# Performance work log

Hardware: AMD Instinct MI355X
Metric: run time of the kernel (lower is better)

## Reference

```python
import jax, jax.numpy as jnp
import numpy as np

C = 256  # in_dims
CQ = C // 2


def setup_inputs() -> dict:
    key = jax.random.key(0)
    ks = jax.random.split(key, 8)
    B, H, W = 8, 64, 64
    x = jax.random.normal(ks[0], (B, C, H, W), dtype=jnp.float32)
    s = 0.02
    Wq = jax.random.normal(ks[1], (CQ, C), dtype=jnp.float32) * s
    bq = jax.random.normal(ks[2], (CQ,), dtype=jnp.float32) * s
    Wk = jax.random.normal(ks[3], (CQ, C), dtype=jnp.float32) * s
    bk = jax.random.normal(ks[4], (CQ,), dtype=jnp.float32) * s
    Wv = jax.random.normal(ks[5], (C, C), dtype=jnp.float32) * s
    bv = jax.random.normal(ks[6], (C,), dtype=jnp.float32) * s
    gamma = jax.random.normal(ks[7], (1,), dtype=jnp.float32) * 0.5  # torch inits to 0; use nonzero for a meaningful test
    return {"x": x, "Wq": Wq, "bq": bq, "Wk": Wk, "bk": bk, "Wv": Wv, "bv": bv, "gamma": gamma}


def reference(x, Wq, bq, Wk, bk, Wv, bv, gamma):
    B, Ch, H, W = x.shape
    N = H * W
    xf = x.reshape(B, Ch, N)  # 1x1 conv == per-pixel linear over channels
    q = jnp.einsum('oc,bcn->bon', Wq, xf) + bq[None, :, None]  # [B, C/2, N]
    k = jnp.einsum('oc,bcn->bon', Wk, xf) + bk[None, :, None]  # [B, C/2, N]
    v = jnp.einsum('oc,bcn->bon', Wv, xf) + bv[None, :, None]  # [B, C,   N]
    # attention[b, m, n] = q_m . k_n ; softmax over dim=1 (the m axis), matching nn.Softmax(dim=1)
    scores = jnp.einsum('bcm,bcn->bmn', q, k)  # [B, N, N]
    attn = jax.nn.softmax(scores, axis=1)
    # torch.bmm(V, A^T)[b,c,m] = sum_n V[b,c,n] * A[b,m,n]
    out = jnp.einsum('bcn,bmn->bcm', v, attn)  # [B, C, N]
    return gamma * out.reshape(B, Ch, H, W) + x
```

## Files before the change

### kernel.cpp

```cpp
#include <hip/hip_runtime.h>


typedef unsigned short u16;
typedef __attribute__((ext_vector_type(8))) short bf16x8;
typedef __attribute__((ext_vector_type(4))) short bf16x4;
typedef __attribute__((ext_vector_type(4))) float f32x4;

__device__ __forceinline__ float bf2f(u16 u) {
  union { unsigned int i; float f; } v; v.i = ((unsigned int)u) << 16; return v.f;
}
__device__ __forceinline__ u16 f2bf(float f) {
  union { float f; unsigned int i; } v; v.f = f;
  unsigned int r = v.i + 0x7fffu + ((v.i >> 16) & 1u);
  return (u16)(r >> 16);
}

#define NB 8
#define NC 256
#define NCQ 128
#define NN 4096
#define LOG2E 1.4426950408889634f

__device__ __forceinline__ int scan_bad(const u16* p, int ns, int tid) {
  int bad = 0;
  for (int i = tid; i < ns; i += 256) {
    const int e = (p[2 * i] >> 7) & 0xff;
    bad |= (e >= 0x90) ? 1 : 0;
  }
  return bad;
}

__device__ __forceinline__ bf16x8 load8(const u16* pb, const float* pf,
                                        size_t off, bool f) {
  if (!f) return *(const bf16x8*)(pb + off);
  const float4 a = *(const float4*)(pf + off);
  const float4 b = *(const float4*)(pf + off + 4);
  bf16x8 r;
  r[0] = (short)f2bf(a.x); r[1] = (short)f2bf(a.y);
  r[2] = (short)f2bf(a.z); r[3] = (short)f2bf(a.w);
  r[4] = (short)f2bf(b.x); r[5] = (short)f2bf(b.y);
  r[6] = (short)f2bf(b.z); r[7] = (short)f2bf(b.w);
  return r;
}

__global__ __launch_bounds__(256, 2) void qkv_kernel(
    const void* xv, const void* Wqv, const void* bqv, const void* Wkv,
    const void* bkv, const void* Wvv, const void* bvv,
    u16* __restrict__ q2T, u16* __restrict__ kT, u16* __restrict__ vout) {
  __shared__ __align__(16) u16 xT[64][264];
  __shared__ int fl[8];
  const int tid = threadIdx.x;
  const int bid = blockIdx.x;
  const int b = bid & 7, n0 = (bid >> 3) << 6;

  if (tid < 8) fl[tid] = 0;
  __syncthreads();
  if (scan_bad((const u16*)xv, 256, tid)) fl[0] = 1;
  if (scan_bad((const u16*)Wqv, 64, tid)) fl[1] = 1;
  if (scan_bad((const u16*)Wkv, 64, tid)) fl[2] = 1;
  if (scan_bad((const u16*)Wvv, 64, tid)) fl[3] = 1;
  if (scan_bad((const u16*)bqv, 64, tid)) fl[4] = 1;
  if (scan_bad((const u16*)bkv, 64, tid)) fl[5] = 1;
  if (scan_bad((const u16*)bvv, 64, tid)) fl[6] = 1;
  __syncthreads();
  const bool fx = fl[0] != 0;

  {
    const int c = tid;
    const size_t roff = (size_t)(b * NC + c) * NN + n0;
    if (fx) {
      const float* xp = (const float*)xv + roff;
#pragma unroll
      for (int j = 0; j < 16; ++j) {
        const float4 t = *(const float4*)(xp + j * 4);
        xT[j * 4 + 0][c] = f2bf(t.x); xT[j * 4 + 1][c] = f2bf(t.y);
        xT[j * 4 + 2][c] = f2bf(t.z); xT[j * 4 + 3][c] = f2bf(t.w);
      }
    } else {
      const u16* xp = (const u16*)xv + roff;
#pragma unroll
      for (int j = 0; j < 8; ++j) {
        bf16x8 t = *(const bf16x8*)(xp + j * 8);
#pragma unroll
        for (int e = 0; e < 8; ++e) xT[j * 8 + e][c] = (u16)t[e];
      }
    }
  }
  __syncthreads();

  const int w = tid >> 6, lane = tid & 63, l15 = lane & 15, quad = lane >> 4;
  const u16* Wb; const float* Wf; const u16* Bb; const float* Bf;
  bool fW, fB; int obase = 0; u16* dstT = nullptr; float sc = 1.f;
  if (w == 0) {
    Wb = (const u16*)Wqv; Wf = (const float*)Wqv;
    Bb = (const u16*)bqv; Bf = (const float*)bqv;
    fW = fl[1]; fB = fl[4]; dstT = q2T; sc = LOG2E;
  } else if (w == 1) {
    Wb = (const u16*)Wkv; Wf = (const float*)Wkv;
    Bb = (const u16*)bkv; Bf = (const float*)bkv;
    fW = fl[2]; fB = fl[5]; dstT = kT;
  } else if (w == 2) {
    Wb = (const u16*)Wvv; Wf = (const float*)Wvv;
    Bb = (const u16*)bvv; Bf = (const float*)bvv;
    fW = fl[3]; fB = fl[6];
  } else {
    Wb = (const u16*)Wvv + 32768; Wf = (const float*)Wvv + 32768;
    Bb = (const u16*)bvv + 128;   Bf = (const float*)bvv + 128;
    fW = fl[3]; fB = fl[6]; obase = 128;
  }

  bf16x8 xfr[4][8];
#pragma unroll
  for (int nt = 0; nt < 4; ++nt) {
    const u16* xp = &xT[nt * 16 + l15][quad * 8];
#pragma unroll
    for (int ks = 0; ks < 8; ++ks) xfr[nt][ks] = *(const bf16x8*)(xp + ks * 32);
  }

  for (int ot = 0; ot < 8; ++ot) {
    bf16x8 wfr[8];
    const size_t wrow = (size_t)(ot * 16 + l15) * 256 + quad * 8;
#pragma unroll
    for (int ks = 0; ks < 8; ++ks) wfr[ks] = load8(Wb, Wf, wrow + ks * 32, fW);
    float bias[4];
    {
      const int boff = ot * 16 + quad * 4;
#pragma unroll
      for (int r = 0; r < 4; ++r)
        bias[r] = fB ? Bf[boff + r] : bf2f(Bb[boff + r]);
    }
#pragma unroll
    for (int nt = 0; nt < 4; ++nt) {
      f32x4 acc = {0.f, 0.f, 0.f, 0.f};
#pragma unroll
      for (int ks = 0; ks < 8; ++ks)
        acc = __builtin_amdgcn_mfma_f32_16x16x32_bf16(wfr[ks], xfr[nt][ks], acc, 0, 0, 0);
      const int n = n0 + nt * 16 + l15;
      if (w < 2) {
        ushort4 st;
        st.x = f2bf((acc[0] + bias[0]) * sc); st.y = f2bf((acc[1] + bias[1]) * sc);
        st.z = f2bf((acc[2] + bias[2]) * sc); st.w = f2bf((acc[3] + bias[3]) * sc);
        *(ushort4*)(dstT + ((size_t)(b * NN + n)) * NCQ + ot * 16 + quad * 4) = st;
      } else {
        const int c = obase + ot * 16 + quad * 4;
#pragma unroll
        for (int r = 0; r < 4; ++r)
          vout[((size_t)(b * NC + c + r)) * NN + n] = f2bf(acc[r] + bias[r]);
      }
    }
  }
}

__global__ __launch_bounds__(256, 2) void stats_kernel(
    const u16* __restrict__ q2T, const u16* __restrict__ kT,
    float* __restrict__ rbuf) {
  __shared__ __align__(16) u16 ksl[64][136];
  __shared__ float zbuf[4][64];
  const int bid = blockIdx.x;
  const int b = bid & 7, n0 = (bid >> 3) << 6;
  const int tid = threadIdx.x;
  const int w = tid >> 6, lane = tid & 63, l15 = lane & 15, quad = lane >> 4;

  {
    const int nn = tid >> 2, ck = (tid & 3) * 32;
    const u16* src = kT + ((size_t)(b * NN + n0 + nn)) * NCQ + ck;
#pragma unroll
    for (int j = 0; j < 4; ++j)
      *(bf16x8*)(&ksl[nn][ck + j * 8]) = *(const bf16x8*)(src + j * 8);
  }
  __syncthreads();

  float Z[4] = {0.f, 0.f, 0.f, 0.f};
  for (int it = 0; it < 64; ++it) {
    const int mb = w * 1024 + it * 16;
    const u16* qp = q2T + ((size_t)(b * NN + mb + l15)) * NCQ + quad * 8;
    bf16x8 af[4];
#pragma unroll
    for (int ks = 0; ks < 4; ++ks) af[ks] = *(const bf16x8*)(qp + ks * 32);
#pragma unroll
    for (int nt = 0; nt < 4; ++nt) {
      f32x4 acc = {0.f, 0.f, 0.f, 0.f};
#pragma unroll
      for (int ks = 0; ks < 4; ++ks) {
        const bf16x8 kfr = *(const bf16x8*)(&ksl[nt * 16 + l15][quad * 8 + ks * 32]);
        acc = __builtin_amdgcn_mfma_f32_16x16x32_bf16(af[ks], kfr, acc, 0, 0, 0);
      }
      Z[nt] += __builtin_amdgcn_exp2f(acc[0]) + __builtin_amdgcn_exp2f(acc[1]) +
               __builtin_amdgcn_exp2f(acc[2]) + __builtin_amdgcn_exp2f(acc[3]);
    }
  }
#pragma unroll
  for (int nt = 0; nt < 4; ++nt) {
    float z = Z[nt];
    z += __shfl_xor(z, 16, 64);
    z += __shfl_xor(z, 32, 64);
    Z[nt] = z;
  }
  if (lane < 16) {
#pragma unroll
    for (int nt = 0; nt < 4; ++nt) zbuf[w][nt * 16 + lane] = Z[nt];
  }
  __syncthreads();
  if (tid < 64) {
    const float z = zbuf[0][tid] + zbuf[1][tid] + zbuf[2][tid] + zbuf[3][tid];
    rbuf[b * NN + n0 + tid] = 1.0f / z;
  }
}

__global__ __launch_bounds__(256, 4) void scale_kernel(
    u16* __restrict__ vr, const float* __restrict__ rbuf) {
  const int flat = (blockIdx.x * 256 + threadIdx.x) * 8;
  const int n = flat & (NN - 1);
  const int b = flat >> 20;
  const float4 r0 = *(const float4*)(rbuf + (b << 12) + n);
  const float4 r1 = *(const float4*)(rbuf + (b << 12) + n + 4);
  const ushort4 a0 = *(const ushort4*)(vr + flat);
  const ushort4 a1 = *(const ushort4*)(vr + flat + 4);
  ushort4 s0, s1;
  s0.x = f2bf(bf2f(a0.x) * r0.x); s0.y = f2bf(bf2f(a0.y) * r0.y);
  s0.z = f2bf(bf2f(a0.z) * r0.z); s0.w = f2bf(bf2f(a0.w) * r0.w);
  s1.x = f2bf(bf2f(a1.x) * r1.x); s1.y = f2bf(bf2f(a1.y) * r1.y);
  s1.z = f2bf(bf2f(a1.z) * r1.z); s1.w = f2bf(bf2f(a1.w) * r1.w);
  *(ushort4*)(vr + flat) = s0;
  *(ushort4*)(vr + flat + 4) = s1;
}

__global__ __launch_bounds__(256, 4) void out_kernel(
    const u16* __restrict__ q2T, const u16* __restrict__ kT,
    const u16* __restrict__ vr,
    const void* xv, const void* gv,
    const void* bqv, const void* bkv, const void* bvv,
    void* outv) {
  __shared__ __align__(16) u16 qs[64][136];
  __shared__ __align__(16) u16 et[2][4][16][68];
  __shared__ int fl[2];
  const int tid = threadIdx.x;
  if (tid < 2) fl[tid] = 0;
  __syncthreads();
  if (scan_bad((const u16*)xv, 256, tid)) fl[0] = 1;
  if (scan_bad((const u16*)bqv, 64, tid) | scan_bad((const u16*)bkv, 64, tid) |
      scan_bad((const u16*)bvv, 64, tid)) fl[1] = 1;

  const int bid = blockIdx.x;
  const int b = bid & 7;
  const int r7 = bid >> 3;
  const int ch = r7 & 1;
  const int m0 = (r7 >> 1) << 6;
  const int w = tid >> 6, lane = tid & 63, l15 = lane & 15, quad = lane >> 4;

  {
    const int mm = tid >> 2, ck = (tid & 3) * 32;
    const u16* src = q2T + ((size_t)(b * NN + m0 + mm)) * NCQ + ck;
#pragma unroll
    for (int j = 0; j < 4; ++j)
      *(bf16x8*)(&qs[mm][ck + j * 8]) = *(const bf16x8*)(src + j * 8);
  }
  __syncthreads();
  const bool fx = fl[0] != 0, fg = fl[1] != 0;

  f32x4 acc[8];
#pragma unroll
  for (int i = 0; i < 8; ++i) acc[i] = (f32x4){0.f, 0.f, 0.f, 0.f};

  const u16* kb = kT + ((size_t)(b * NN + w * 16 + l15)) * NCQ + quad * 8;
  const u16* vb = vr + ((size_t)(b * NC + ch * 128 + w * 32 + l15)) * NN + quad * 8;

  for (int n0 = 0; n0 < NN; n0 += 64) {
    const int pp = (n0 >> 6) & 1;
    bf16x8 kf[4], vf[4];
#pragma unroll
    for (int ks = 0; ks < 4; ++ks)
      kf[ks] = *(const bf16x8*)(kb + (size_t)n0 * NCQ + ks * 32);
#pragma unroll
    for (int ct = 0; ct < 2; ++ct)
#pragma unroll
      for (int ns = 0; ns < 2; ++ns)
        vf[ct * 2 + ns] =
            *(const bf16x8*)(vb + (size_t)(ct * 16) * NN + n0 + ns * 32);
#pragma unroll
    for (int mg = 0; mg < 4; ++mg) {
      f32x4 s = {0.f, 0.f, 0.f, 0.f};
#pragma unroll
      for (int ks = 0; ks < 4; ++ks) {
        const bf16x8 qfr =
            *(const bf16x8*)(&qs[mg * 16 + l15][quad * 8 + ks * 32]);
        s = __builtin_amdgcn_mfma_f32_16x16x32_bf16(kf[ks], qfr, s, 0, 0, 0);
      }
      bf16x4 ev;
      ev[0] = (short)f2bf(__builtin_amdgcn_exp2f(s[0]));
      ev[1] = (short)f2bf(__builtin_amdgcn_exp2f(s[1]));
      ev[2] = (short)f2bf(__builtin_amdgcn_exp2f(s[2]));
      ev[3] = (short)f2bf(__builtin_amdgcn_exp2f(s[3]));
      *(bf16x4*)(&et[pp][mg][l15][w * 16 + quad * 4]) = ev;
    }
    __syncthreads();
#pragma unroll
    for (int mg = 0; mg < 4; ++mg)
#pragma unroll
      for (int ns = 0; ns < 2; ++ns) {
        const bf16x8 af = *(const bf16x8*)(&et[pp][mg][l15][ns * 32 + quad * 8]);
#pragma unroll
        for (int ct = 0; ct < 2; ++ct)
          acc[mg * 2 + ct] = __builtin_amdgcn_mfma_f32_16x16x32_bf16(
              af, vf[ct * 2 + ns], acc[mg * 2 + ct], 0, 0, 0);
      }
  }

  const float g = fg ? ((const float*)gv)[0] : bf2f(((const u16*)gv)[0]);
#pragma unroll
  for (int mg = 0; mg < 4; ++mg)
#pragma unroll
    for (int ct = 0; ct < 2; ++ct) {
      const int c = ch * 128 + w * 32 + ct * 16 + l15;
      const int m = m0 + mg * 16 + quad * 4;
      const size_t base = ((size_t)(b * NC + c)) * NN + m;
      const f32x4 a = acc[mg * 2 + ct];
      if (fx) {
        const float4 xl = *(const float4*)((const float*)xv + base);
        float4 st;
        st.x = g * a[0] + xl.x; st.y = g * a[1] + xl.y;
        st.z = g * a[2] + xl.z; st.w = g * a[3] + xl.w;
        *(float4*)((float*)outv + base) = st;
      } else {
        const ushort4 xl = *(const ushort4*)((const u16*)xv + base);
        ushort4 st;
        st.x = f2bf(g * a[0] + bf2f(xl.x));
        st.y = f2bf(g * a[1] + bf2f(xl.y));
        st.z = f2bf(g * a[2] + bf2f(xl.z));
        st.w = f2bf(g * a[3] + bf2f(xl.w));
        *(ushort4*)((u16*)outv + base) = st;
      }
    }
}

extern "C" void kernel_launch(void* const* d_in, const int* in_sizes, int n_in,
                              void* d_out, int out_size, void* d_ws, size_t ws_size,
                              hipStream_t stream) {
  const size_t NEED = 33554432u;
  if (ws_size < NEED) return;

  char* ws = (char*)d_ws;
  u16* q2 = (u16*)(ws);
  u16* kk = (u16*)(ws + 8388608);
  u16* vv = (u16*)(ws + 16777216);
  float* rbuf = (ws_size >= NEED + 131072u) ? (float*)(ws + NEED) : (float*)d_out;

  qkv_kernel<<<512, 256, 0, stream>>>(d_in[0], d_in[1], d_in[2], d_in[3],
                                      d_in[4], d_in[5], d_in[6], q2, kk, vv);
  stats_kernel<<<512, 256, 0, stream>>>(q2, kk, rbuf);
  scale_kernel<<<4096, 256, 0, stream>>>(vv, rbuf);
  out_kernel<<<1024, 256, 0, stream>>>(q2, kk, vv, d_in[0], d_in[7],
                                       d_in[2], d_in[4], d_in[6], d_out);
}
```

Before: 432.7 us.

## Software-pipeline K/V and Q loads with register double-buffering and lighter barriers

The output kernel now unrolls its key loop by two and holds two register sets for K and V fragments, so the global loads for the next 64-key tile are issued before the barrier and overlap the current tile's MFMA and exp work. The full __syncthreads is replaced by a barrier that waits only on LDS counters, so outstanding global loads are not drained at each barrier. The stats kernel likewise prefetches the next Q fragments one iteration ahead, and the LDS row padding drops from 136 to 132 elements to change bank mapping. The extra register buffers raise VGPR pressure and may cut occupancy, and the last prefetch wraps around to a redundant load.

New measurement: 437.2 us. About the same (+1.0%).

```diff
diff --git a/kernel.cpp b/kernel.cpp
--- a/kernel.cpp
+++ b/kernel.cpp
@@ -13,6 +13,13 @@
   union { float f; unsigned int i; } v; v.f = f;
   unsigned int r = v.i + 0x7fffu + ((v.i >> 16) & 1u);
   return (u16)(r >> 16);
+}
+
+__device__ __forceinline__ void lgkm_barrier() {
+  __asm__ __volatile__("" ::: "memory");
+  __builtin_amdgcn_s_waitcnt(0xC07F);
+  __builtin_amdgcn_s_barrier();
+  __asm__ __volatile__("" ::: "memory");
 }
 
 #define NB 8
@@ -20,6 +27,7 @@
 #define NCQ 128
 #define NN 4096
 #define LOG2E 1.4426950408889634f
+#define QS_STRIDE 132
 
 __device__ __forceinline__ int scan_bad(const u16* p, int ns, int tid) {
   int bad = 0;
@@ -154,7 +162,7 @@
 __global__ __launch_bounds__(256, 2) void stats_kernel(
     const u16* __restrict__ q2T, const u16* __restrict__ kT,
     float* __restrict__ rbuf) {
-  __shared__ __align__(16) u16 ksl[64][136];
+  __shared__ __align__(16) u16 ksl[64][QS_STRIDE];
   __shared__ float zbuf[4][64];
   const int bid = blockIdx.x;
   const int b = bid & 7, n0 = (bid >> 3) << 6;
@@ -170,24 +178,31 @@
   }
   __syncthreads();
 
+  const u16* qbase = q2T + ((size_t)(b * NN + w * 1024 + l15)) * NCQ + quad * 8;
+  bf16x8 af[4], afN[4];
+#pragma unroll
+  for (int ks = 0; ks < 4; ++ks) af[ks] = *(const bf16x8*)(qbase + ks * 32);
+
   float Z[4] = {0.f, 0.f, 0.f, 0.f};
   for (int it = 0; it < 64; ++it) {
-    const int mb = w * 1024 + it * 16;
-    const u16* qp = q2T + ((size_t)(b * NN + mb + l15)) * NCQ + quad * 8;
-    bf16x8 af[4];
-#pragma unroll
-    for (int ks = 0; ks < 4; ++ks) af[ks] = *(const bf16x8*)(qp + ks * 32);
+    const int itn = (it + 1) & 63;
+    const u16* qpn = qbase + (size_t)(itn * 16) * NCQ;
+#pragma unroll
+    for (int ks = 0; ks < 4; ++ks) afN[ks] = *(const bf16x8*)(qpn + ks * 32);
 #pragma unroll
     for (int nt = 0; nt < 4; ++nt) {
       f32x4 acc = {0.f, 0.f, 0.f, 0.f};
 #pragma unroll
       for (int ks = 0; ks < 4; ++ks) {
-        const bf16x8 kfr = *(const bf16x8*)(&ksl[nt * 16 + l15][quad * 8 + ks * 32]);
+        const bf16x8 kfr =
+            *(const bf16x8*)(&ksl[nt * 16 + l15][quad * 8 + ks * 32]);
         acc = __builtin_amdgcn_mfma_f32_16x16x32_bf16(af[ks], kfr, acc, 0, 0, 0);
       }
       Z[nt] += __builtin_amdgcn_exp2f(acc[0]) + __builtin_amdgcn_exp2f(acc[1]) +
                __builtin_amdgcn_exp2f(acc[2]) + __builtin_amdgcn_exp2f(acc[3]);
     }
+#pragma unroll
+    for (int ks = 0; ks < 4; ++ks) af[ks] = afN[ks];
   }
 #pragma unroll
   for (int nt = 0; nt < 4; ++nt) {
@@ -225,13 +240,53 @@
   *(ushort4*)(vr + flat + 4) = s1;
 }
 
+#define K3_S_PHASE(KF, PP)                                                    \
+  {                                                                           \
+    _Pragma("unroll") for (int mg = 0; mg < 4; ++mg) {                        \
+      f32x4 s = {0.f, 0.f, 0.f, 0.f};                                         \
+      _Pragma("unroll") for (int ks = 0; ks < 4; ++ks) {                      \
+        const bf16x8 qfr =                                                    \
+            *(const bf16x8*)(&qs[mg * 16 + l15][quad * 8 + ks * 32]);         \
+        s = __builtin_amdgcn_mfma_f32_16x16x32_bf16(KF[ks], qfr, s, 0, 0, 0); \
+      }                                                                       \
+      bf16x4 ev;                                                              \
+      ev[0] = (short)f2bf(__builtin_amdgcn_exp2f(s[0]));                      \
+      ev[1] = (short)f2bf(__builtin_amdgcn_exp2f(s[1]));                      \
+      ev[2] = (short)f2bf(__builtin_amdgcn_exp2f(s[2]));                      \
+      ev[3] = (short)f2bf(__builtin_amdgcn_exp2f(s[3]));                      \
+      *(bf16x4*)(&et[PP][mg][l15][w * 16 + quad * 4]) = ev;                   \
+    }                                                                         \
+  }
+
+#define K3_LOADS(KF, VF, NX)                                                  \
+  {                                                                           \
+    const int nx = (NX) & (NN - 1);                                           \
+    _Pragma("unroll") for (int ks = 0; ks < 4; ++ks)                          \
+        KF[ks] = *(const bf16x8*)(kb + (size_t)nx * NCQ + ks * 32);           \
+    _Pragma("unroll") for (int ct = 0; ct < 2; ++ct)                          \
+        _Pragma("unroll") for (int ns = 0; ns < 2; ++ns)                      \
+            VF[ct * 2 + ns] =                                                 \
+        *(const bf16x8*)(vb + (size_t)(ct * 16) * NN + nx + ns * 32);         \
+  }
+
+#define K3_PV_PHASE(VF, PP)                                                   \
+  {                                                                           \
+    _Pragma("unroll") for (int mg = 0; mg < 4; ++mg)                          \
+        _Pragma("unroll") for (int ns = 0; ns < 2; ++ns) {                    \
+      const bf16x8 af = *(const bf16x8*)(&et[PP][mg][l15][ns * 32 + quad * 8]); \
+      _Pragma("unroll") for (int ct = 0; ct < 2; ++ct)                        \
+          acc[mg * 2 + ct] = __builtin_amdgcn_mfma_f32_16x16x32_bf16(         \
+              af, VF[ct * 2 + ns], acc[mg * 2 + ct], 0, 0, 0);                \
+    }                                                                         \
+  }
+
 __global__ __launch_bounds__(256, 4) void out_kernel(
     const u16* __restrict__ q2T, const u16* __restrict__ kT,
     const u16* __restrict__ vr,
     const void* xv, const void* gv,
     const void* bqv, const void* bkv, const void* bvv,
     void* outv) {
-  __shared__ __align__(16) u16 qs[64][136];
+  __shared__ __align__(16) u16 qs[64][QS_STRIDE];
   __shared__ __align__(16) u16 et[2][4][16][68];
   __shared__ int fl[2];
   const int tid = threadIdx.x;
@@ -265,45 +320,18 @@
   const u16* kb = kT + ((size_t)(b * NN + w * 16 + l15)) * NCQ + quad * 8;
   const u16* vb = vr + ((size_t)(b * NC + ch * 128 + w * 32 + l15)) * NN + quad * 8;
 
-  for (int n0 = 0; n0 < NN; n0 += 64) {
-    const int pp = (n0 >> 6) & 1;
-    bf16x8 kf[4], vf[4];
-#pragma unroll
-    for (int ks = 0; ks < 4; ++ks)
-      kf[ks] = *(const bf16x8*)(kb + (size_t)n0 * NCQ + ks * 32);
-#pragma unroll
-    for (int ct = 0; ct < 2; ++ct)
-#pragma unroll
-      for (int ns = 0; ns < 2; ++ns)
-        vf[ct * 2 + ns] =
-            *(const bf16x8*)(vb + (size_t)(ct * 16) * NN + n0 + ns * 32);
-#pragma unroll
-    for (int mg = 0; mg < 4; ++mg) {
-      f32x4 s = {0.f, 0.f, 0.f, 0.f};
-#pragma unroll
-      for (int ks = 0; ks < 4; ++ks) {
-        const bf16x8 qfr =
-            *(const bf16x8*)(&qs[mg * 16 + l15][quad * 8 + ks * 32]);
-        s = __builtin_amdgcn_mfma_f32_16x16x32_bf16(kf[ks], qfr, s, 0, 0, 0);
-      }
-      bf16x4 ev;
-      ev[0] = (short)f2bf(__builtin_amdgcn_exp2f(s[0]));
-      ev[1] = (short)f2bf(__builtin_amdgcn_exp2f(s[1]));
-      ev[2] = (short)f2bf(__builtin_amdgcn_exp2f(s[2]));
-      ev[3] = (short)f2bf(__builtin_amdgcn_exp2f(s[3]));
-      *(bf16x4*)(&et[pp][mg][l15][w * 16 + quad * 4]) = ev;
-    }
-    __syncthreads();
-#pragma unroll
-    for (int mg = 0; mg < 4; ++mg)
-#pragma unroll
-      for (int ns = 0; ns < 2; ++ns) {
-        const bf16x8 af = *(const bf16x8*)(&et[pp][mg][l15][ns * 32 + quad * 8]);
-#pragma unroll
-        for (int ct = 0; ct < 2; ++ct)
-          acc[mg * 2 + ct] = __builtin_amdgcn_mfma_f32_16x16x32_bf16(
-              af, vf[ct * 2 + ns], acc[mg * 2 + ct], 0, 0, 0);
-      }
+  bf16x8 kfA[4], vfA[4], kfB[4], vfB[4];
+  K3_LOADS(kfA, vfA, 0);
+
+  for (int n0 = 0; n0 < NN; n0 += 128) {
+    K3_S_PHASE(kfA, 0)
+    K3_LOADS(kfB, vfB, n0 + 64)
+    lgkm_barrier();
+    K3_PV_PHASE(vfA, 0)
+    K3_S_PHASE(kfB, 1)
+    K3_LOADS(kfA, vfA, n0 + 128)
+    lgkm_barrier();
+    K3_PV_PHASE(vfB, 1)
   }
 
   const float g = fg ? ((const float*)gv)[0] : bf2f(((const u16*)gv)[0]);
```
